# Kernel optimization log

Hardware: AMD Instinct MI355X
Metric: run time of the kernel (lower is better)

The kernel has to match this reference:

```python
import jax, jax.numpy as jnp
import numpy as np

T = 16384
IN = 14
H = 100
OUT = 1


def setup_inputs() -> dict:
    key = jax.random.key(0)
    ks = jax.random.split(key, 11)
    s_in = 1.0 / np.sqrt(H)
    x = jax.random.normal(ks[0], (T, IN), dtype=jnp.float32)
    # PyTorch nn.GRU params: weight_ih_l{k} [3H, in], weight_hh_l{k} [3H, H], biases [3H]; gate order (r, z, n)
    w_ih0 = jax.random.uniform(ks[1], (3 * H, IN), minval=-s_in, maxval=s_in, dtype=jnp.float32)
    w_hh0 = jax.random.uniform(ks[2], (3 * H, H), minval=-s_in, maxval=s_in, dtype=jnp.float32)
    b_ih0 = jax.random.uniform(ks[3], (3 * H,), minval=-s_in, maxval=s_in, dtype=jnp.float32)
    b_hh0 = jax.random.uniform(ks[4], (3 * H,), minval=-s_in, maxval=s_in, dtype=jnp.float32)
    w_ih1 = jax.random.uniform(ks[5], (3 * H, H), minval=-s_in, maxval=s_in, dtype=jnp.float32)
    w_hh1 = jax.random.uniform(ks[6], (3 * H, H), minval=-s_in, maxval=s_in, dtype=jnp.float32)
    b_ih1 = jax.random.uniform(ks[7], (3 * H,), minval=-s_in, maxval=s_in, dtype=jnp.float32)
    b_hh1 = jax.random.uniform(ks[8], (3 * H,), minval=-s_in, maxval=s_in, dtype=jnp.float32)
    fc_w = jax.random.uniform(ks[9], (OUT, H), minval=-s_in, maxval=s_in, dtype=jnp.float32)
    fc_b = jax.random.uniform(ks[10], (OUT,), minval=-s_in, maxval=s_in, dtype=jnp.float32)
    return {"x": x, "w_ih0": w_ih0, "w_hh0": w_hh0, "b_ih0": b_ih0, "b_hh0": b_hh0,
            "w_ih1": w_ih1, "w_hh1": w_hh1, "b_ih1": b_ih1, "b_hh1": b_hh1,
            "fc_w": fc_w, "fc_b": fc_b}


def _gru_layer(x_seq, w_ih, w_hh, b_ih, b_hh):
    # x_seq: [T, D_in] (batch=1 squeezed). Precompute input projections for all steps.
    gi = x_seq @ w_ih.T + b_ih  # [T, 3H]

    def step(h, gi_t):
        gh = h @ w_hh.T + b_hh  # [3H]
        i_r, i_z, i_n = jnp.split(gi_t, 3)
        h_r, h_z, h_n = jnp.split(gh, 3)
        r = jax.nn.sigmoid(i_r + h_r)
        z = jax.nn.sigmoid(i_z + h_z)
        n = jnp.tanh(i_n + r * h_n)
        h_new = (1.0 - z) * n + z * h
        return h_new, h_new

    h0 = jnp.zeros((w_hh.shape[1],), dtype=x_seq.dtype)
    _, out = jax.lax.scan(step, h0, gi)
    return out  # [T, H]


def reference(x, w_ih0, w_hh0, b_ih0, b_hh0, w_ih1, w_hh1, b_ih1, b_hh1, fc_w, fc_b):
    h1 = _gru_layer(x, w_ih0, w_hh0, b_ih0, b_hh0)   # layer 0: [T, H]
    h2 = _gru_layer(h1, w_ih1, w_hh1, b_ih1, b_hh1)  # layer 1: [T, H]
    out = h2 @ fc_w.T + fc_b                          # [T, 1]
    return out[-1]                                     # [1]
```

## Files before the change

### kernel.cpp

```cpp
#include <hip/hip_runtime.h>
#include <math.h>

#define T_STEPS 16384
#define IN_DIM  14
#define H_DIM   100
#define G_DIM   300

typedef float f2 __attribute__((ext_vector_type(2)));

#define REP25(M) M(0) M(1) M(2) M(3) M(4) M(5) M(6) M(7) M(8) M(9) M(10) M(11) \
                 M(12) M(13) M(14) M(15) M(16) M(17) M(18) M(19) M(20) M(21) M(22) M(23) M(24)

__global__ void gi0_kernel(const float* __restrict__ x,
                           const float* __restrict__ w_ih0,
                           const float* __restrict__ b_ih0,
                           float* __restrict__ gi0) {
    int e = blockIdx.x * blockDim.x + threadIdx.x;
    if (e >= T_STEPS * G_DIM) return;
    int t = e / G_DIM;
    int j = e - t * G_DIM;
    const float* xr = x + t * IN_DIM;
    const float* wr = w_ih0 + j * IN_DIM;
    float acc = b_ih0[j];
    #pragma unroll
    for (int k = 0; k < IN_DIM; ++k) acc = fmaf(xr[k], wr[k], acc);
    gi0[e] = acc;
}

__global__ __launch_bounds__(512, 2)
void gru_seq_kernel(const float* __restrict__ gi0,
                    const float* __restrict__ w_hh0,
                    const float* __restrict__ b_hh0,
                    const float* __restrict__ w_ih1,
                    const float* __restrict__ b_ih1,
                    const float* __restrict__ w_hh1,
                    const float* __restrict__ b_hh1,
                    const float* __restrict__ fc_w,
                    const float* __restrict__ fc_b,
                    float* __restrict__ out) {
    __shared__ __align__(16) float hbuf[256];
    __shared__ __align__(16) float gh[3 * G_DIM];

    const int tid = threadIdx.x;
    const int idx = (tid < 450) ? tid : 449;
    const int g   = idx / 150;
    const int pr  = idx - g * 150;
    const int r0  = 2 * pr;
    const bool active = (tid < 450);

    const float* wbase; const float* bbase;
    if (g == 0)      { wbase = w_hh0; bbase = b_hh0; }
    else if (g == 1) { wbase = w_ih1; bbase = b_ih1; }
    else             { wbase = w_hh1; bbase = b_hh1; }
    const float bias0 = bbase[r0];
    const float bias1 = bbase[r0 + 1];
    const int hoff4 = (g == 2) ? 32 : 0;
    const int ghw   = (g * G_DIM) / 2 + pr;

    #define DECLK(k) f2 w0a_##k, w0b_##k, w1a_##k, w1b_##k;
    REP25(DECLK)
    #undef DECLK
    {
        const float4* p0 = reinterpret_cast<const float4*>(wbase + (size_t)r0 * H_DIM);
        const float4* p1 = reinterpret_cast<const float4*>(wbase + (size_t)(r0 + 1) * H_DIM);
        #define LOADK(k) { float4 A = p0[k]; w0a_##k.x = A.x; w0a_##k.y = A.y; w0b_##k.x = A.z; w0b_##k.y = A.w; \
                           float4 B = p1[k]; w1a_##k.x = B.x; w1a_##k.y = B.y; w1b_##k.x = B.z; w1b_##k.y = B.w; }
        REP25(LOADK)
        #undef LOADK
    }

    if (tid < 256) hbuf[tid] = 0.0f;
    __syncthreads();

    const float4* hb4 = reinterpret_cast<const float4*>(hbuf);
    float2* gh2 = reinterpret_cast<float2*>(gh);

    for (int i = 0; i <= T_STEPS; ++i) {
        float gr = 0.f, gz = 0.f, gn = 0.f;
        if (tid < H_DIM && i < T_STEPS) {
            const float* p = gi0 + (size_t)i * G_DIM + tid;
            gr = p[0]; gz = p[H_DIM]; gn = p[2 * H_DIM];
        }

        f2 acc0, acc1, acc2, acc3;
        acc0.x = bias0; acc0.y = 0.0f;
        acc1.x = 0.0f;  acc1.y = 0.0f;
        acc2.x = bias1; acc2.y = 0.0f;
        acc3.x = 0.0f;  acc3.y = 0.0f;
        #define DOTK(k) { float4 V = hb4[hoff4 + k]; \
                          f2 va, vb; va.x = V.x; va.y = V.y; vb.x = V.z; vb.y = V.w; \
                          acc0 += w0a_##k * va; acc1 += w0b_##k * vb; \
                          acc2 += w1a_##k * va; acc3 += w1b_##k * vb; }
        REP25(DOTK)
        #undef DOTK
        if (active) {
            float a = (acc0.x + acc1.x) + (acc0.y + acc1.y);
            float b = (acc2.x + acc3.x) + (acc2.y + acc3.y);
            gh2[ghw] = make_float2(a, b);
        }
        __syncthreads();

        if (tid < H_DIM) {
            if (i < T_STEPS) {
                float r = 1.0f / (1.0f + expf(-(gr + gh[tid])));
                float z = 1.0f / (1.0f + expf(-(gz + gh[H_DIM + tid])));
                float n = tanhf(gn + r * gh[2 * H_DIM + tid]);
                float hp = hbuf[tid];
                hbuf[tid] = (1.0f - z) * n + z * hp;
            }
        } else if (tid >= 256 && tid < 256 + H_DIM) {
            if (i >= 1) {
                int j = tid - 256;
                float r = 1.0f / (1.0f + expf(-(gh[G_DIM + j] + gh[2 * G_DIM + j])));
                float z = 1.0f / (1.0f + expf(-(gh[G_DIM + H_DIM + j] + gh[2 * G_DIM + H_DIM + j])));
                float n = tanhf(gh[G_DIM + 2 * H_DIM + j] + r * gh[2 * G_DIM + 2 * H_DIM + j]);
                float hp = hbuf[128 + j];
                hbuf[128 + j] = (1.0f - z) * n + z * hp;
            }
        }
        __syncthreads();
    }

    if (tid < 64) {
        float s = 0.0f;
        for (int j = tid; j < H_DIM; j += 64) s = fmaf(fc_w[j], hbuf[128 + j], s);
        #pragma unroll
        for (int off = 32; off > 0; off >>= 1) s += __shfl_down(s, off);
        if (tid == 0) out[0] = s + fc_b[0];
    }
}

extern "C" void kernel_launch(void* const* d_in, const int* in_sizes, int n_in,
                              void* d_out, int out_size, void* d_ws, size_t ws_size,
                              hipStream_t stream) {
    const float* x     = (const float*)d_in[0];
    const float* w_ih0 = (const float*)d_in[1];
    const float* w_hh0 = (const float*)d_in[2];
    const float* b_ih0 = (const float*)d_in[3];
    const float* b_hh0 = (const float*)d_in[4];
    const float* w_ih1 = (const float*)d_in[5];
    const float* w_hh1 = (const float*)d_in[6];
    const float* b_ih1 = (const float*)d_in[7];
    const float* b_hh1 = (const float*)d_in[8];
    const float* fc_w  = (const float*)d_in[9];
    const float* fc_b  = (const float*)d_in[10];
    float* out = (float*)d_out;
    float* gi0 = (float*)d_ws;

    const int total = T_STEPS * G_DIM;
    gi0_kernel<<<(total + 255) / 256, 256, 0, stream>>>(x, w_ih0, b_ih0, gi0);
    gru_seq_kernel<<<1, 512, 0, stream>>>(gi0, w_hh0, b_hh0, w_ih1, b_ih1,
                                          w_hh1, b_hh1, fc_w, fc_b, out);
}
```

Baseline: 15.68 ms.

## Double-buffer hidden state and fuse gate math into dot-product waves, one barrier per step

```diff
diff --git a/kernel.cpp b/kernel.cpp
--- a/kernel.cpp
+++ b/kernel.cpp
@@ -5,6 +5,10 @@
 #define IN_DIM  14
 #define H_DIM   100
 #define G_DIM   300
+
+#define H1OFF 0
+#define H2OFF 128
+#define AOFF  256
 
 typedef float f2 __attribute__((ext_vector_type(2)));
 
@@ -38,92 +42,125 @@
                     const float* __restrict__ fc_w,
                     const float* __restrict__ fc_b,
                     float* __restrict__ out) {
-    __shared__ __align__(16) float hbuf[256];
-    __shared__ __align__(16) float gh[3 * G_DIM];
+    __shared__ __align__(16) float bufA[1024];
+    __shared__ __align__(16) float bufB[1024];
 
     const int tid = threadIdx.x;
-    const int idx = (tid < 450) ? tid : 449;
-    const int g   = idx / 150;
-    const int pr  = idx - g * 150;
-    const int r0  = 2 * pr;
-    const bool active = (tid < 450);
+    const int wv = tid >> 6;
+    const int ln = tid & 63;
+    const bool gateWave = (tid < 320);
 
-    const float* wbase; const float* bbase;
-    if (g == 0)      { wbase = w_hh0; bbase = b_hh0; }
-    else if (g == 1) { wbase = w_ih1; bbase = b_ih1; }
-    else             { wbase = w_hh1; bbase = b_hh1; }
-    const float bias0 = bbase[r0];
-    const float bias1 = bbase[r0 + 1];
-    const int hoff4 = (g == 2) ? 32 : 0;
-    const int ghw   = (g * G_DIM) / 2 + pr;
+    const float* pra; const float* prb; float bias0, bias1;
+    int hbase4 = 0;
+    bool isA = false;
+    int gg = 0;
+    int jw = 0;
+
+    if (gateWave) {
+        if (ln < 40) {
+            isA = true;
+            gg = wv * 40 + ln;
+            int gl = (gg < 100) ? gg : gg - 100;
+            const float* wm = (gg < 100) ? w_hh0 : w_hh1;
+            const float* bm = (gg < 100) ? b_hh0 : b_hh1;
+            pra = wm + (size_t)gl * H_DIM;
+            prb = wm + (size_t)(gl + 100) * H_DIM;
+            bias0 = bm[gl]; bias1 = bm[gl + 100];
+            hbase4 = (gg < 100) ? (H1OFF / 4) : (H2OFF / 4);
+            jw = gl;
+        } else {
+            int b = (ln < 60) ? (ln - 40) : 19;
+            int pb = wv * 40 + 2 * b;
+            int gl = (pb < 100) ? pb : pb - 100;
+            const float* wm = (pb < 100) ? w_hh0 : w_hh1;
+            const float* bm = (pb < 100) ? b_hh0 : b_hh1;
+            pra = wm + (size_t)(200 + gl) * H_DIM;
+            prb = wm + (size_t)(201 + gl) * H_DIM;
+            bias0 = bm[200 + gl]; bias1 = bm[201 + gl];
+            hbase4 = (pb < 100) ? (H1OFF / 4) : (H2OFF / 4);
+        }
+    } else {
+        int s = tid - 320;
+        int q = (s < 150) ? s : 149;
+        pra = w_ih1 + (size_t)(2 * q) * H_DIM;
+        prb = w_ih1 + (size_t)(2 * q + 1) * H_DIM;
+        bias0 = b_ih1[2 * q]; bias1 = b_ih1[2 * q + 1];
+        hbase4 = H1OFF / 4;
+        jw = q;
+    }
+    const bool l1inActive = (!gateWave) && (tid - 320 < 150);
+    const int hsoff = hbase4 << 2;
 
     #define DECLK(k) f2 w0a_##k, w0b_##k, w1a_##k, w1b_##k;
     REP25(DECLK)
     #undef DECLK
     {
-        const float4* p0 = reinterpret_cast<const float4*>(wbase + (size_t)r0 * H_DIM);
-        const float4* p1 = reinterpret_cast<const float4*>(wbase + (size_t)(r0 + 1) * H_DIM);
+        const float4* p0 = reinterpret_cast<const float4*>(pra);
+        const float4* p1 = reinterpret_cast<const float4*>(prb);
         #define LOADK(k) { float4 A = p0[k]; w0a_##k.x = A.x; w0a_##k.y = A.y; w0b_##k.x = A.z; w0b_##k.y = A.w; \
                            float4 B = p1[k]; w1a_##k.x = B.x; w1a_##k.y = B.y; w1b_##k.x = B.z; w1b_##k.y = B.w; }
         REP25(LOADK)
         #undef LOADK
     }
 
-    if (tid < 256) hbuf[tid] = 0.0f;
+    for (int k = tid; k < 1024; k += 512) { bufA[k] = 0.0f; bufB[k] = 0.0f; }
     __syncthreads();
 
-    const float4* hb4 = reinterpret_cast<const float4*>(hbuf);
-    float2* gh2 = reinterpret_cast<float2*>(gh);
+    for (int it = 0; it < T_STEPS + 2; ++it) {
+        float* bc = (it & 1) ? bufB : bufA;
+        float* bn = (it & 1) ? bufA : bufB;
 
-    for (int i = 0; i <= T_STEPS; ++i) {
-        float gr = 0.f, gz = 0.f, gn = 0.f;
-        if (tid < H_DIM && i < T_STEPS) {
-            const float* p = gi0 + (size_t)i * G_DIM + tid;
-            gr = p[0]; gz = p[H_DIM]; gn = p[2 * H_DIM];
+        float gr = 0.f, gz = 0.f, gn = 0.f, hold = 0.f;
+        if (isA) {
+            if (gg < 100) {
+                if (it < T_STEPS) {
+                    const float* p = gi0 + (size_t)it * G_DIM + jw;
+                    gr = p[0]; gz = p[H_DIM]; gn = p[2 * H_DIM];
+                }
+            } else {
+                gr = bc[AOFF + jw];
+                gz = bc[AOFF + 100 + jw];
+                gn = bc[AOFF + 200 + jw];
+            }
+            hold = bc[hsoff + jw];
         }
 
+        const float4* hb4 = reinterpret_cast<const float4*>(bc) + hbase4;
         f2 acc0, acc1, acc2, acc3;
         acc0.x = bias0; acc0.y = 0.0f;
         acc1.x = 0.0f;  acc1.y = 0.0f;
         acc2.x = bias1; acc2.y = 0.0f;
         acc3.x = 0.0f;  acc3.y = 0.0f;
-        #define DOTK(k) { float4 V = hb4[hoff4 + k]; \
+        #define DOTK(k) { float4 V = hb4[k]; \
                           f2 va, vb; va.x = V.x; va.y = V.y; vb.x = V.z; vb.y = V.w; \
                           acc0 += w0a_##k * va; acc1 += w0b_##k * vb; \
                           acc2 += w1a_##k * va; acc3 += w1b_##k * vb; }
         REP25(DOTK)
         #undef DOTK
-        if (active) {
-            float a = (acc0.x + acc1.x) + (acc0.y + acc1.y);
-            float b = (acc2.x + acc3.x) + (acc2.y + acc3.y);
-            gh2[ghw] = make_float2(a, b);
-        }
-        __syncthreads();
+        float d0 = (acc0.x + acc1.x) + (acc0.y + acc1.y);
+        float d1 = (acc2.x + acc3.x) + (acc2.y + acc3.y);
 
-        if (tid < H_DIM) {
-            if (i < T_STEPS) {
-                float r = 1.0f / (1.0f + expf(-(gr + gh[tid])));
-                float z = 1.0f / (1.0f + expf(-(gz + gh[H_DIM + tid])));
-                float n = tanhf(gn + r * gh[2 * H_DIM + tid]);
-                float hp = hbuf[tid];
-                hbuf[tid] = (1.0f - z) * n + z * hp;
+        if (gateWave) {
+            int src = (40 + (ln >> 1)) << 2;
+            float nh0 = __int_as_float(__builtin_amdgcn_ds_bpermute(src, __float_as_int(d0)));
+            float nh1 = __int_as_float(__builtin_amdgcn_ds_bpermute(src, __float_as_int(d1)));
+            float nh = (ln & 1) ? nh1 : nh0;
+            bool act = isA && ((gg < 100) ? (it < T_STEPS) : (it >= 2));
+            if (act) {
+                float r = 1.0f / (1.0f + expf(-(gr + d0)));
+                float z = 1.0f / (1.0f + expf(-(gz + d1)));
+                float n = tanhf(gn + r * nh);
+                bn[hsoff + jw] = (1.0f - z) * n + z * hold;
             }
-        } else if (tid >= 256 && tid < 256 + H_DIM) {
-            if (i >= 1) {
-                int j = tid - 256;
-                float r = 1.0f / (1.0f + expf(-(gh[G_DIM + j] + gh[2 * G_DIM + j])));
-                float z = 1.0f / (1.0f + expf(-(gh[G_DIM + H_DIM + j] + gh[2 * G_DIM + H_DIM + j])));
-                float n = tanhf(gh[G_DIM + 2 * H_DIM + j] + r * gh[2 * G_DIM + 2 * H_DIM + j]);
-                float hp = hbuf[128 + j];
-                hbuf[128 + j] = (1.0f - z) * n + z * hp;
-            }
+        } else if (l1inActive && it >= 1 && it <= T_STEPS) {
+            reinterpret_cast<float2*>(bn + AOFF)[jw] = make_float2(d0, d1);
         }
         __syncthreads();
     }
 
     if (tid < 64) {
         float s = 0.0f;
-        for (int j = tid; j < H_DIM; j += 64) s = fmaf(fc_w[j], hbuf[128 + j], s);
+        for (int j = tid; j < H_DIM; j += 64) s = fmaf(fc_w[j], bufA[H2OFF + j], s);
         #pragma unroll
         for (int off = 32; off > 0; off >>= 1) s += __shfl_down(s, off);
         if (tid == 0) out[0] = s + fc_b[0];
```

Result: no change. 15.50 ms (-1.2%).

## Pipeline GRU layers with one barrier per step using double-buffered shared state

Applied to the files above, without the earlier changes.

```diff
diff --git a/kernel.cpp b/kernel.cpp
--- a/kernel.cpp
+++ b/kernel.cpp
@@ -6,7 +6,12 @@
 #define H_DIM   100
 #define G_DIM   300
 
+#define H1OFF 0
+#define H2OFF 132
+#define AOFF  256
+
 typedef float f2 __attribute__((ext_vector_type(2)));
+typedef float f4 __attribute__((ext_vector_type(4)));
 
 #define REP25(M) M(0) M(1) M(2) M(3) M(4) M(5) M(6) M(7) M(8) M(9) M(10) M(11) \
                  M(12) M(13) M(14) M(15) M(16) M(17) M(18) M(19) M(20) M(21) M(22) M(23) M(24)
@@ -27,7 +32,7 @@
     gi0[e] = acc;
 }
 
-__global__ __launch_bounds__(512, 2)
+__global__ __launch_bounds__(256, 1)
 void gru_seq_kernel(const float* __restrict__ gi0,
                     const float* __restrict__ w_hh0,
                     const float* __restrict__ b_hh0,
@@ -38,92 +43,123 @@
                     const float* __restrict__ fc_w,
                     const float* __restrict__ fc_b,
                     float* __restrict__ out) {
-    __shared__ __align__(16) float hbuf[256];
-    __shared__ __align__(16) float gh[3 * G_DIM];
+    __shared__ __align__(16) float bufA[1024];
+    __shared__ __align__(16) float bufB[1024];
 
     const int tid = threadIdx.x;
-    const int idx = (tid < 450) ? tid : 449;
-    const int g   = idx / 150;
-    const int pr  = idx - g * 150;
-    const int r0  = 2 * pr;
-    const bool active = (tid < 450);
 
-    const float* wbase; const float* bbase;
-    if (g == 0)      { wbase = w_hh0; bbase = b_hh0; }
-    else if (g == 1) { wbase = w_ih1; bbase = b_ih1; }
-    else             { wbase = w_hh1; bbase = b_hh1; }
-    const float bias0 = bbase[r0];
-    const float bias1 = bbase[r0 + 1];
-    const int hoff4 = (g == 2) ? 32 : 0;
-    const int ghw   = (g * G_DIM) / 2 + pr;
+    const float *r0p, *r1p, *r2p, *r3p;
+    float b0, b1, b2, b3;
+    int hoff4, j;
+    if (tid < 100) {
+        j = tid;
+        r0p = w_hh0 + (size_t)j * H_DIM;
+        r1p = w_hh0 + (size_t)(j + 100) * H_DIM;
+        r2p = w_hh0 + (size_t)(j + 200) * H_DIM;
+        r3p = w_ih1 + (size_t)j * H_DIM;
+        b0 = b_hh0[j]; b1 = b_hh0[j + 100]; b2 = b_hh0[j + 200]; b3 = b_ih1[j];
+        hoff4 = H1OFF / 4;
+    } else if (tid < 200) {
+        j = tid - 100;
+        r0p = w_hh1 + (size_t)j * H_DIM;
+        r1p = w_hh1 + (size_t)(j + 100) * H_DIM;
+        r2p = w_hh1 + (size_t)(j + 200) * H_DIM;
+        r3p = r0p;
+        b0 = b_hh1[j]; b1 = b_hh1[j + 100]; b2 = b_hh1[j + 200]; b3 = 0.0f;
+        hoff4 = H2OFF / 4;
+    } else {
+        int m = tid - 200; if (m > 49) m = 49;
+        j = m;
+        r0p = w_ih1 + (size_t)(100 + 4 * m)     * H_DIM;
+        r1p = w_ih1 + (size_t)(100 + 4 * m + 1) * H_DIM;
+        r2p = w_ih1 + (size_t)(100 + 4 * m + 2) * H_DIM;
+        r3p = w_ih1 + (size_t)(100 + 4 * m + 3) * H_DIM;
+        b0 = b_ih1[100 + 4 * m];     b1 = b_ih1[100 + 4 * m + 1];
+        b2 = b_ih1[100 + 4 * m + 2]; b3 = b_ih1[100 + 4 * m + 3];
+        hoff4 = H1OFF / 4;
+    }
 
-    #define DECLK(k) f2 w0a_##k, w0b_##k, w1a_##k, w1b_##k;
+    #define DECLK(k) f2 wa0_##k, wb0_##k, wa1_##k, wb1_##k, wa2_##k, wb2_##k, wa3_##k, wb3_##k;
     REP25(DECLK)
     #undef DECLK
     {
-        const float4* p0 = reinterpret_cast<const float4*>(wbase + (size_t)r0 * H_DIM);
-        const float4* p1 = reinterpret_cast<const float4*>(wbase + (size_t)(r0 + 1) * H_DIM);
-        #define LOADK(k) { float4 A = p0[k]; w0a_##k.x = A.x; w0a_##k.y = A.y; w0b_##k.x = A.z; w0b_##k.y = A.w; \
-                           float4 B = p1[k]; w1a_##k.x = B.x; w1a_##k.y = B.y; w1b_##k.x = B.z; w1b_##k.y = B.w; }
+        const f4* p0 = reinterpret_cast<const f4*>(r0p);
+        const f4* p1 = reinterpret_cast<const f4*>(r1p);
+        const f4* p2 = reinterpret_cast<const f4*>(r2p);
+        const f4* p3 = reinterpret_cast<const f4*>(r3p);
+        #define LOADK(k) { f4 V; V = p0[k]; wa0_##k = V.lo; wb0_##k = V.hi; \
+                           V = p1[k]; wa1_##k = V.lo; wb1_##k = V.hi; \
+                           V = p2[k]; wa2_##k = V.lo; wb2_##k = V.hi; \
+                           V = p3[k]; wa3_##k = V.lo; wb3_##k = V.hi; }
         REP25(LOADK)
         #undef LOADK
     }
 
-    if (tid < 256) hbuf[tid] = 0.0f;
+    for (int k = tid; k < 1024; k += 256) { bufA[k] = 0.0f; bufB[k] = 0.0f; }
     __syncthreads();
 
-    const float4* hb4 = reinterpret_cast<const float4*>(hbuf);
-    float2* gh2 = reinterpret_cast<float2*>(gh);
+    for (int it = 0; it < T_STEPS + 2; ++it) {
+        float* bc = (it & 1) ? bufB : bufA;
+        float* bn = (it & 1) ? bufA : bufB;
 
-    for (int i = 0; i <= T_STEPS; ++i) {
-        float gr = 0.f, gz = 0.f, gn = 0.f;
-        if (tid < H_DIM && i < T_STEPS) {
-            const float* p = gi0 + (size_t)i * G_DIM + tid;
-            gr = p[0]; gz = p[H_DIM]; gn = p[2 * H_DIM];
+        float gr = 0.f, gz = 0.f, gn = 0.f, hold = 0.f;
+        if (tid < 100) {
+            if (it < T_STEPS) {
+                const float* p = gi0 + (size_t)it * G_DIM + tid;
+                gr = p[0]; gz = p[H_DIM]; gn = p[2 * H_DIM];
+            }
+            hold = bc[H1OFF + tid];
+        } else if (tid < 200) {
+            gr = bc[AOFF + j];
+            gz = bc[AOFF + 100 + j];
+            gn = bc[AOFF + 200 + j];
+            hold = bc[H2OFF + j];
         }
 
-        f2 acc0, acc1, acc2, acc3;
-        acc0.x = bias0; acc0.y = 0.0f;
-        acc1.x = 0.0f;  acc1.y = 0.0f;
-        acc2.x = bias1; acc2.y = 0.0f;
-        acc3.x = 0.0f;  acc3.y = 0.0f;
-        #define DOTK(k) { float4 V = hb4[hoff4 + k]; \
-                          f2 va, vb; va.x = V.x; va.y = V.y; vb.x = V.z; vb.y = V.w; \
-                          acc0 += w0a_##k * va; acc1 += w0b_##k * vb; \
-                          acc2 += w1a_##k * va; acc3 += w1b_##k * vb; }
+        const f4* hb4 = reinterpret_cast<const f4*>(bc) + hoff4;
+        f2 a0A, a0B, a1A, a1B, a2A, a2B, a3A, a3B;
+        a0A.x = b0; a0A.y = 0.0f;  a0B.x = 0.0f; a0B.y = 0.0f;
+        a1A.x = b1; a1A.y = 0.0f;  a1B.x = 0.0f; a1B.y = 0.0f;
+        a2A.x = b2; a2A.y = 0.0f;  a2B.x = 0.0f; a2B.y = 0.0f;
+        a3A.x = b3; a3A.y = 0.0f;  a3B.x = 0.0f; a3B.y = 0.0f;
+        #define DOTK(k) { f4 V = hb4[k]; f2 lo = V.lo, hi = V.hi; \
+                          a0A += wa0_##k * lo; a0B += wb0_##k * hi; \
+                          a1A += wa1_##k * lo; a1B += wb1_##k * hi; \
+                          a2A += wa2_##k * lo; a2B += wb2_##k * hi; \
+                          a3A += wa3_##k * lo; a3B += wb3_##k * hi; }
         REP25(DOTK)
         #undef DOTK
-        if (active) {
-            float a = (acc0.x + acc1.x) + (acc0.y + acc1.y);
-            float b = (acc2.x + acc3.x) + (acc2.y + acc3.y);
-            gh2[ghw] = make_float2(a, b);
-        }
-        __syncthreads();
+        float d0 = (a0A.x + a0B.x) + (a0A.y + a0B.y);
+        float d1 = (a1A.x + a1B.x) + (a1A.y + a1B.y);
+        float d2 = (a2A.x + a2B.x) + (a2A.y + a2B.y);
+        float d3 = (a3A.x + a3B.x) + (a3A.y + a3B.y);
 
-        if (tid < H_DIM) {
-            if (i < T_STEPS) {
-                float r = 1.0f / (1.0f + expf(-(gr + gh[tid])));
-                float z = 1.0f / (1.0f + expf(-(gz + gh[H_DIM + tid])));
-                float n = tanhf(gn + r * gh[2 * H_DIM + tid]);
-                float hp = hbuf[tid];
-                hbuf[tid] = (1.0f - z) * n + z * hp;
+        if (tid < 100) {
+            if (it < T_STEPS) {
+                float r = 1.0f / (1.0f + expf(-(gr + d0)));
+                float z = 1.0f / (1.0f + expf(-(gz + d1)));
+                float n = tanhf(gn + r * d2);
+                bn[H1OFF + tid] = (1.0f - z) * n + z * hold;
             }
-        } else if (tid >= 256 && tid < 256 + H_DIM) {
-            if (i >= 1) {
-                int j = tid - 256;
-                float r = 1.0f / (1.0f + expf(-(gh[G_DIM + j] + gh[2 * G_DIM + j])));
-                float z = 1.0f / (1.0f + expf(-(gh[G_DIM + H_DIM + j] + gh[2 * G_DIM + H_DIM + j])));
-                float n = tanhf(gh[G_DIM + 2 * H_DIM + j] + r * gh[2 * G_DIM + 2 * H_DIM + j]);
-                float hp = hbuf[128 + j];
-                hbuf[128 + j] = (1.0f - z) * n + z * hp;
+            if (it >= 1 && it <= T_STEPS)
+                bn[AOFF + tid] = d3;
+        } else if (tid < 200) {
+            if (it >= 2) {
+                float r = 1.0f / (1.0f + expf(-(gr + d0)));
+                float z = 1.0f / (1.0f + expf(-(gz + d1)));
+                float n = tanhf(gn + r * d2);
+                bn[H2OFF + j] = (1.0f - z) * n + z * hold;
             }
+        } else if (tid < 250 && it >= 1 && it <= T_STEPS) {
+            f4 w; w.x = d0; w.y = d1; w.z = d2; w.w = d3;
+            reinterpret_cast<f4*>(bn + AOFF + 100)[j] = w;
         }
         __syncthreads();
     }
 
     if (tid < 64) {
         float s = 0.0f;
-        for (int j = tid; j < H_DIM; j += 64) s = fmaf(fc_w[j], hbuf[128 + j], s);
+        for (int k = tid; k < H_DIM; k += 64) s = fmaf(fc_w[k], bufA[H2OFF + k], s);
         #pragma unroll
         for (int off = 32; off > 0; off >>= 1) s += __shfl_down(s, off);
         if (tid == 0) out[0] = s + fc_b[0];
@@ -149,6 +185,6 @@
 
     const int total = T_STEPS * G_DIM;
     gi0_kernel<<<(total + 255) / 256, 256, 0, stream>>>(x, w_ih0, b_ih0, gi0);
-    gru_seq_kernel<<<1, 512, 0, stream>>>(gi0, w_hh0, b_hh0, w_ih1, b_ih1,
+    gru_seq_kernel<<<1, 256, 0, stream>>>(gi0, w_hh0, b_hh0, w_ih1, b_ih1,
                                           w_hh1, b_hh1, fc_w, fc_b, out);
 }
```

New measurement: 30.99 ms. 1.98x slower.

## Pipeline GRU layers across 1024 threads with double-buffered LDS and one barrier per step

Applied to the files above, without the earlier changes.

```diff
diff --git a/kernel.cpp b/kernel.cpp
--- a/kernel.cpp
+++ b/kernel.cpp
@@ -6,7 +6,12 @@
 #define H_DIM   100
 #define G_DIM   300
 
+#define H1OFF 0
+#define H2OFF 132
+#define AOFF  256
+
 typedef float f2 __attribute__((ext_vector_type(2)));
+typedef float f4 __attribute__((ext_vector_type(4)));
 
 #define REP25(M) M(0) M(1) M(2) M(3) M(4) M(5) M(6) M(7) M(8) M(9) M(10) M(11) \
                  M(12) M(13) M(14) M(15) M(16) M(17) M(18) M(19) M(20) M(21) M(22) M(23) M(24)
@@ -27,7 +32,7 @@
     gi0[e] = acc;
 }
 
-__global__ __launch_bounds__(512, 2)
+__global__ __launch_bounds__(1024, 4)
 void gru_seq_kernel(const float* __restrict__ gi0,
                     const float* __restrict__ w_hh0,
                     const float* __restrict__ b_hh0,
@@ -38,84 +43,95 @@
                     const float* __restrict__ fc_w,
                     const float* __restrict__ fc_b,
                     float* __restrict__ out) {
-    __shared__ __align__(16) float hbuf[256];
-    __shared__ __align__(16) float gh[3 * G_DIM];
+    __shared__ __align__(16) float bufA[1024];
+    __shared__ __align__(16) float bufB[1024];
 
     const int tid = threadIdx.x;
-    const int idx = (tid < 450) ? tid : 449;
-    const int g   = idx / 150;
-    const int pr  = idx - g * 150;
-    const int r0  = 2 * pr;
-    const bool active = (tid < 450);
+    const int wave = tid >> 6;
+    const int ln = tid & 63;
 
-    const float* wbase; const float* bbase;
-    if (g == 0)      { wbase = w_hh0; bbase = b_hh0; }
-    else if (g == 1) { wbase = w_ih1; bbase = b_ih1; }
-    else             { wbase = w_hh1; bbase = b_hh1; }
-    const float bias0 = bbase[r0];
-    const float bias1 = bbase[r0 + 1];
-    const int hoff4 = (g == 2) ? 32 : 0;
-    const int ghw   = (g * G_DIM) / 2 + pr;
+    int grp, gbase;
+    if (wave < 5)       { grp = 0; gbase = wave * 20; }
+    else if (wave < 10) { grp = 1; gbase = (wave - 5) * 20; }
+    else if (wave < 15) { grp = 2; gbase = (wave - 10) * 20; }
+    else                { grp = 3; gbase = 0; }
 
-    #define DECLK(k) f2 w0a_##k, w0b_##k, w1a_##k, w1b_##k;
+    const int ln20 = ln % 20;
+    const int role = ln / 20;
+    const int roleC = (role > 2) ? 2 : role;
+    const int q = gbase + ln20;
+    const int row = roleC * 100 + q;
+    const bool isR = (role == 0);
+
+    const float* wm; const float* bm;
+    if (grp == 0)      { wm = w_hh0; bm = b_hh0; }
+    else if (grp == 1) { wm = w_hh1; bm = b_hh1; }
+    else if (grp == 2) { wm = w_ih1; bm = b_ih1; }
+    else               { wm = w_hh0; bm = b_hh0; }
+    const int rowE = (grp == 3) ? 0 : row;
+    const float bias = (grp == 3) ? 0.0f : bm[rowE];
+    const int hoff  = (grp == 1) ? H2OFF : H1OFF;
+    const int hoff4 = hoff / 4;
+
+    const int adZ = (20 + ln20) << 2;
+    const int adN = (40 + ln20) << 2;
+
+    #define DECLK(k) f2 wa_##k, wb_##k;
     REP25(DECLK)
     #undef DECLK
     {
-        const float4* p0 = reinterpret_cast<const float4*>(wbase + (size_t)r0 * H_DIM);
-        const float4* p1 = reinterpret_cast<const float4*>(wbase + (size_t)(r0 + 1) * H_DIM);
-        #define LOADK(k) { float4 A = p0[k]; w0a_##k.x = A.x; w0a_##k.y = A.y; w0b_##k.x = A.z; w0b_##k.y = A.w; \
-                           float4 B = p1[k]; w1a_##k.x = B.x; w1a_##k.y = B.y; w1b_##k.x = B.z; w1b_##k.y = B.w; }
+        const f4* p = reinterpret_cast<const f4*>(wm + (size_t)rowE * H_DIM);
+        #define LOADK(k) { f4 V = p[k]; wa_##k = V.lo; wb_##k = V.hi; }
         REP25(LOADK)
         #undef LOADK
     }
 
-    if (tid < 256) hbuf[tid] = 0.0f;
+    for (int k = tid; k < 1024; k += 1024) { }
+    if (tid < 1024) { bufA[tid] = 0.0f; bufB[tid] = 0.0f; }
     __syncthreads();
 
-    const float4* hb4 = reinterpret_cast<const float4*>(hbuf);
-    float2* gh2 = reinterpret_cast<float2*>(gh);
+    for (int it = 0; it < T_STEPS + 2; ++it) {
+        float* bc = (it & 1) ? bufB : bufA;
+        float* bn = (it & 1) ? bufA : bufB;
 
-    for (int i = 0; i <= T_STEPS; ++i) {
-        float gr = 0.f, gz = 0.f, gn = 0.f;
-        if (tid < H_DIM && i < T_STEPS) {
-            const float* p = gi0 + (size_t)i * G_DIM + tid;
-            gr = p[0]; gz = p[H_DIM]; gn = p[2 * H_DIM];
-        }
+        if (grp < 3) {
+            float g_r = 0.f, g_z = 0.f, g_n = 0.f, hold = 0.f;
+            if (grp == 0) {
+                if (isR && it < T_STEPS) {
+                    const float* p = gi0 + (size_t)it * G_DIM + q;
+                    g_r = p[0]; g_z = p[H_DIM]; g_n = p[2 * H_DIM];
+                }
+                if (isR) hold = bc[H1OFF + q];
+            } else if (grp == 1) {
+                if (isR) {
+                    g_r  = bc[AOFF + q];
+                    g_z  = bc[AOFF + 100 + q];
+                    g_n  = bc[AOFF + 200 + q];
+                    hold = bc[H2OFF + q];
+                }
+            }
 
-        f2 acc0, acc1, acc2, acc3;
-        acc0.x = bias0; acc0.y = 0.0f;
-        acc1.x = 0.0f;  acc1.y = 0.0f;
-        acc2.x = bias1; acc2.y = 0.0f;
-        acc3.x = 0.0f;  acc3.y = 0.0f;
-        #define DOTK(k) { float4 V = hb4[hoff4 + k]; \
-                          f2 va, vb; va.x = V.x; va.y = V.y; vb.x = V.z; vb.y = V.w; \
-                          acc0 += w0a_##k * va; acc1 += w0b_##k * vb; \
-                          acc2 += w1a_##k * va; acc3 += w1b_##k * vb; }
-        REP25(DOTK)
-        #undef DOTK
-        if (active) {
-            float a = (acc0.x + acc1.x) + (acc0.y + acc1.y);
-            float b = (acc2.x + acc3.x) + (acc2.y + acc3.y);
-            gh2[ghw] = make_float2(a, b);
-        }
-        __syncthreads();
+            const f4* hb4 = reinterpret_cast<const f4*>(bc) + hoff4;
+            f2 accA, accB;
+            accA.x = bias; accA.y = 0.0f;
+            accB.x = 0.0f; accB.y = 0.0f;
+            #define DOTK(k) { f4 V = hb4[k]; accA += wa_##k * V.lo; accB += wb_##k * V.hi; }
+            REP25(DOTK)
+            #undef DOTK
+            float d = (accA.x + accB.x) + (accA.y + accB.y);
 
-        if (tid < H_DIM) {
-            if (i < T_STEPS) {
-                float r = 1.0f / (1.0f + expf(-(gr + gh[tid])));
-                float z = 1.0f / (1.0f + expf(-(gz + gh[H_DIM + tid])));
-                float n = tanhf(gn + r * gh[2 * H_DIM + tid]);
-                float hp = hbuf[tid];
-                hbuf[tid] = (1.0f - z) * n + z * hp;
-            }
-        } else if (tid >= 256 && tid < 256 + H_DIM) {
-            if (i >= 1) {
-                int j = tid - 256;
-                float r = 1.0f / (1.0f + expf(-(gh[G_DIM + j] + gh[2 * G_DIM + j])));
-                float z = 1.0f / (1.0f + expf(-(gh[G_DIM + H_DIM + j] + gh[2 * G_DIM + H_DIM + j])));
-                float n = tanhf(gh[G_DIM + 2 * H_DIM + j] + r * gh[2 * G_DIM + 2 * H_DIM + j]);
-                float hp = hbuf[128 + j];
-                hbuf[128 + j] = (1.0f - z) * n + z * hp;
+            if (grp <= 1) {
+                float dz = __int_as_float(__builtin_amdgcn_ds_bpermute(adZ, __float_as_int(d)));
+                float dn = __int_as_float(__builtin_amdgcn_ds_bpermute(adN, __float_as_int(d)));
+                bool act = isR && ((grp == 0) ? (it < T_STEPS) : (it >= 2));
+                if (act) {
+                    float r = 1.0f / (1.0f + expf(-(g_r + d)));
+                    float z = 1.0f / (1.0f + expf(-(g_z + dz)));
+                    float n = tanhf(g_n + r * dn);
+                    bn[hoff + q] = (1.0f - z) * n + z * hold;
+                }
+            } else {
+                if (role < 3 && it >= 1 && it <= T_STEPS) bn[AOFF + row] = d;
             }
         }
         __syncthreads();
@@ -123,7 +139,7 @@
 
     if (tid < 64) {
         float s = 0.0f;
-        for (int j = tid; j < H_DIM; j += 64) s = fmaf(fc_w[j], hbuf[128 + j], s);
+        for (int k = tid; k < H_DIM; k += 64) s = fmaf(fc_w[k], bufA[H2OFF + k], s);
         #pragma unroll
         for (int off = 32; off > 0; off >>= 1) s += __shfl_down(s, off);
         if (tid == 0) out[0] = s + fc_b[0];
@@ -149,6 +165,6 @@
 
     const int total = T_STEPS * G_DIM;
     gi0_kernel<<<(total + 255) / 256, 256, 0, stream>>>(x, w_ih0, b_ih0, gi0);
-    gru_seq_kernel<<<1, 512, 0, stream>>>(gi0, w_hh0, b_hh0, w_ih1, b_ih1,
-                                          w_hh1, b_hh1, fc_w, fc_b, out);
+    gru_seq_kernel<<<1, 1024, 0, stream>>>(gi0, w_hh0, b_hh0, w_ih1, b_ih1,
+                                           w_hh1, b_hh1, fc_w, fc_b, out);
 }
```

Measured after the change: 21.15 ms. 34.9% more time.
